# Optimization experiments

Hardware: AMD Instinct MI355X
Metric: run time of the kernel (lower is better)

The kernel has to match this reference:

```python
import jax, jax.numpy as jnp
import numpy as np

B, T, D = 64, 512, 128          # batch, time, input_dim
S = 16                           # num_sessions
P, STRIDE = 3, 1                 # patch size / stride
H = 512                          # hidden_size
HORIZONS = (1, 5, 10)
K = len(HORIZONS)
TOK = D * P                      # token_dim = 384
EPS = 1e-6


def setup_inputs() -> dict:
    key = jax.random.key(0)
    ks = jax.random.split(key, 16)
    s = 0.02
    return {
        "x": jax.random.normal(ks[0], (B, T, D), jnp.float32),
        "session_idx": jax.random.randint(ks[1], (B,), 0, S),
        # per-session affine (expert) params
        "sess_W": jax.random.normal(ks[2], (S, D, D), jnp.float32) * s,
        "sess_b": jax.random.normal(ks[3], (S, D), jnp.float32) * s,
        # projection token_dim -> hidden
        "proj_W": jax.random.normal(ks[4], (H, TOK), jnp.float32) * s,
        "proj_b": jax.random.normal(ks[5], (H,), jnp.float32) * s,
        "rms_scale": jnp.ones((H,), jnp.float32),
        # single-layer GRU params (PyTorch layout: [3H, in], gate order r,z,n)
        "gru_Wih": jax.random.normal(ks[6], (3 * H, H), jnp.float32) * s,
        "gru_Whh": jax.random.normal(ks[7], (3 * H, H), jnp.float32) * s,
        "gru_bih": jax.random.normal(ks[8], (3 * H,), jnp.float32) * s,
        "gru_bhh": jax.random.normal(ks[9], (3 * H,), jnp.float32) * s,
        # future heads (K horizons): Linear(H,H) -> GELU -> Linear(H,TOK)
        "head_W1": jax.random.normal(ks[10], (K, H, H), jnp.float32) * s,
        "head_b1": jax.random.normal(ks[11], (K, H), jnp.float32) * s,
        "head_W2": jax.random.normal(ks[12], (K, TOK, H), jnp.float32) * s,
        "head_b2": jax.random.normal(ks[13], (K, TOK), jnp.float32) * s,
    }


def _forward(x, session_idx, sess_W, sess_b, proj_W, proj_b, rms_scale,
             gru_Wih, gru_Whh, gru_bih, gru_bhh,
             head_W1, head_b1, head_W2, head_b2):
    # --- per-sample session affine (expert gather + batched GEMM) ---
    W = sess_W[session_idx]                      # [B, D, D]
    b = sess_b[session_idx]                      # [B, D]
    aligned = jnp.einsum('btd,bed->bte', x, W) + b[:, None, :]  # y = x @ W.T + b

    # --- patch unfold along time; torch unfold gives [N, D, P] -> flatten (d,p) ---
    N = (T - P) // STRIDE + 1
    idx = jnp.arange(N)[:, None] * STRIDE + jnp.arange(P)[None, :]  # [N, P]
    win = aligned[:, idx, :]                     # [B, N, P, D]
    tokens = jnp.transpose(win, (0, 1, 3, 2)).reshape(B, N, TOK)    # [B, N, D*P]

    # --- projection + RMSNorm ---
    h = tokens @ proj_W.T + proj_b               # [B, N, H]
    rms = jnp.sqrt(jnp.mean(h * h, axis=-1, keepdims=True) + EPS)
    h = h / rms * rms_scale

    # --- GRU (PyTorch gate order r, z, n) via lax.scan over time ---
    gx = h @ gru_Wih.T + gru_bih                 # [B, N, 3H], precomputed input gates
    gx_t = jnp.transpose(gx, (1, 0, 2))          # [N, B, 3H]

    def step(hprev, g):
        gh = hprev @ gru_Whh.T + gru_bhh         # [B, 3H]
        r = jax.nn.sigmoid(g[:, :H] + gh[:, :H])
        z = jax.nn.sigmoid(g[:, H:2 * H] + gh[:, H:2 * H])
        n = jnp.tanh(g[:, 2 * H:] + r * gh[:, 2 * H:])
        hn = (1.0 - z) * n + z * hprev
        return hn, hn

    h0 = jnp.zeros((B, H), h.dtype)
    _, hs = jax.lax.scan(step, h0, gx_t)         # [N, B, H]
    hidden = jnp.transpose(hs, (1, 0, 2))        # [B, N, H]

    # --- multi-head future MLPs (stacked over K horizons) ---
    a = jnp.einsum('bnh,kfh->kbnf', hidden, head_W1) + head_b1[:, None, None, :]
    a = jax.nn.gelu(a, approximate=False)        # torch nn.GELU default = exact
    preds = jnp.einsum('kbnf,ktf->kbnt', a, head_W2) + head_b2[:, None, None, :]
    return preds, tokens                          # preds: [K, B, N, TOK]


def reference(x, session_idx, sess_W, sess_b, proj_W, proj_b, rms_scale,
              gru_Wih, gru_Whh, gru_bih, gru_bhh,
              head_W1, head_b1, head_W2, head_b2):
    return _forward(x, session_idx, sess_W, sess_b, proj_W, proj_b, rms_scale,
                    gru_Wih, gru_Whh, gru_bih, gru_bhh,
                    head_W1, head_b1, head_W2, head_b2)
```

## Files before the change

kernel.cpp:

```cpp
#include <hip/hip_runtime.h>
#include <hip/hip_bf16.h>
#include <math.h>

typedef __hip_bfloat16 bf16;
typedef __attribute__((ext_vector_type(8))) short short8;
typedef __attribute__((ext_vector_type(4))) short short4v;
typedef __attribute__((ext_vector_type(4))) float f32x4;

#define B_    64
#define T_    512
#define D_    128
#define N_    510
#define H_    512
#define TOK_  384
#define PRED1_ 12533760L
#define TOKOFF_ 37601280L

#define O_XBF  0UL
#define O_SWB  8388608UL
#define O_PW   8912896UL
#define O_WIH  9306112UL
#define O_WHH  10878976UL
#define O_W1   12451840UL
#define O_W2   14024704UL
#define O_TOK  15204352UL
#define O_HBF  40271872UL
#define O_HID  73695232UL
#define O_ABF  107118592UL
#define O_GX   140541952UL

__global__ void k_f2b(const float* __restrict__ s, bf16* __restrict__ d, int n4) {
  int i = blockIdx.x * 256 + threadIdx.x;
  if (i < n4) {
    float4 v = ((const float4*)s)[i];
    union { short4v sv; bf16 h[4]; } u;
    u.h[0] = __float2bfloat16(v.x); u.h[1] = __float2bfloat16(v.y);
    u.h[2] = __float2bfloat16(v.z); u.h[3] = __float2bfloat16(v.w);
    ((short4v*)d)[i] = u.sv;
  }
}

enum { EPI_F32 = 0, EPI_BF16 = 1, EPI_GELU = 2, EPI_TOK = 3, EPI_F32R = 4 };
#define SLDA 40

template <int EPI>
__global__ __launch_bounds__(256, 2) void k_gemm(
    const bf16* __restrict__ A, const bf16* __restrict__ W,
    const float* __restrict__ bias, void* __restrict__ C,
    int K, int ldc, long zA, long zW, long zB, long zC,
    const int* __restrict__ sidx, float* __restrict__ tokf, bf16* __restrict__ tokb)
{
  const int tid = threadIdx.x;
  const int bm = blockIdx.x, bn = blockIdx.y, z = blockIdx.z;
  const int wsel = (EPI == EPI_TOK) ? sidx[z] : z;
  const int lane = tid & 63, wave = tid >> 6;
  const int wm = (wave & 1) << 6, wn = (wave >> 1) << 6;
  const int r16 = lane & 15, quad = lane >> 4;

  __shared__ bf16 sA[128 * SLDA];
  __shared__ bf16 sB[128 * SLDA];

  const bf16* Ag = A + (long)z * zA + (long)bm * 128 * K;
  const bf16* Wg = W + (long)wsel * zW + (long)bn * 128 * K;

  f32x4 zf = {0.f, 0.f, 0.f, 0.f};
  f32x4 acc[4][4];
  for (int i = 0; i < 4; ++i) for (int j = 0; j < 4; ++j) acc[i][j] = zf;

  const int sr = tid >> 1, sc = (tid & 1) << 4;
  for (int k0 = 0; k0 < K; k0 += 32) {
    *(short8*)&sA[sr*SLDA + sc]     = *(const short8*)&Ag[(long)sr*K + k0 + sc];
    *(short8*)&sA[sr*SLDA + sc + 8] = *(const short8*)&Ag[(long)sr*K + k0 + sc + 8];
    *(short8*)&sB[sr*SLDA + sc]     = *(const short8*)&Wg[(long)sr*K + k0 + sc];
    *(short8*)&sB[sr*SLDA + sc + 8] = *(const short8*)&Wg[(long)sr*K + k0 + sc + 8];
    __syncthreads();
    short8 fa[4], fb[4];
    for (int i = 0; i < 4; ++i) fa[i] = *(const short8*)&sA[(wm + i*16 + r16)*SLDA + quad*8];
    for (int j = 0; j < 4; ++j) fb[j] = *(const short8*)&sB[(wn + j*16 + r16)*SLDA + quad*8];
    for (int i = 0; i < 4; ++i)
      for (int j = 0; j < 4; ++j)
        acc[i][j] = __builtin_amdgcn_mfma_f32_16x16x32_bf16(fa[i], fb[j], acc[i][j], 0, 0, 0);
    __syncthreads();
  }

  const float* bz = bias + (long)wsel * zB + bn * 128;
  for (int i = 0; i < 4; ++i) {
    for (int j = 0; j < 4; ++j) {
      const int colL = wn + j*16 + r16;
      const float bv = bz[colL];
      for (int r = 0; r < 4; ++r) {
        float v = acc[i][j][r] + bv;
        const long grow = (long)bm*128 + wm + i*16 + quad*4 + r;
        const long gcol = (long)bn*128 + colL;
        if (EPI == EPI_F32) {
          ((float*)C)[(long)z*zC + grow*ldc + gcol] = v;
        } else if (EPI == EPI_BF16) {
          ((bf16*)C)[(long)z*zC + grow*ldc + gcol] = __float2bfloat16(v);
        } else if (EPI == EPI_GELU) {
          v = 0.5f * v * (1.0f + erff(v * 0.70710678118654752f));
          ((bf16*)C)[(long)z*zC + grow*ldc + gcol] = __float2bfloat16(v);
        } else if (EPI == EPI_F32R) {
          const long rb = grow & 63, rn = grow >> 6;
          ((float*)C)[(rb*510 + rn)*ldc + gcol] = v;
        } else {
          for (int p = 0; p < 3; ++p) {
            long n = grow - p;
            if (n >= 0 && n < N_) {
              tokf[((long)z*N_ + n)*TOK_ + gcol*3 + p] = v;
              tokb[((long)n*B_ + z)*TOK_ + gcol*3 + p] = __float2bfloat16(v);
            }
          }
        }
      }
    }
  }
}

__global__ __launch_bounds__(256) void k_rms(const float* __restrict__ hpre,
                                             const float* __restrict__ scale,
                                             bf16* __restrict__ hbf)
{
  const int wave = threadIdx.x >> 6, lane = threadIdx.x & 63;
  const long row = (long)blockIdx.x * 4 + wave;
  const float* p = hpre + row * 512 + lane * 8;
  float4 v0 = *(const float4*)p;
  float4 v1 = *(const float4*)(p + 4);
  float ss = v0.x*v0.x + v0.y*v0.y + v0.z*v0.z + v0.w*v0.w
           + v1.x*v1.x + v1.y*v1.y + v1.z*v1.z + v1.w*v1.w;
  for (int m = 32; m >= 1; m >>= 1) ss += __shfl_xor(ss, m, 64);
  const float inv = 1.0f / sqrtf(ss * (1.0f/512.0f) + 1e-6f);
  const float* sc = scale + lane * 8;
  union { short8 sv; bf16 h[8]; } u;
  u.h[0] = __float2bfloat16(v0.x*inv*sc[0]); u.h[1] = __float2bfloat16(v0.y*inv*sc[1]);
  u.h[2] = __float2bfloat16(v0.z*inv*sc[2]); u.h[3] = __float2bfloat16(v0.w*inv*sc[3]);
  u.h[4] = __float2bfloat16(v1.x*inv*sc[4]); u.h[5] = __float2bfloat16(v1.y*inv*sc[5]);
  u.h[6] = __float2bfloat16(v1.z*inv*sc[6]); u.h[7] = __float2bfloat16(v1.w*inv*sc[7]);
  *(short8*)(hbf + row * 512 + lane * 8) = u.sv;
}

#define KP 520

__global__ __launch_bounds__(64, 1) void k_gru(
    const bf16* __restrict__ gx,
    const bf16* __restrict__ Whh,
    const float* __restrict__ bhh,
    bf16* __restrict__ hidden,
    int* __restrict__ flags)
{
  const int lane = threadIdx.x & 63;
  const int c16  = lane & 15, quad = lane >> 4;
  const int pw   = blockIdx.x & 31;
  const int gb   = blockIdx.x >> 5;
  const int hwv  = pw * 16;
  const int b0   = gb * 8;

  __shared__ bf16 wlds[3 * 16 * KP];

  for (int rr = 0; rr < 48; ++rr) {
    const int g3 = rr >> 4, r = rr & 15;
    *(short8*)&wlds[(g3*16 + r)*KP + lane*8] =
        *(const short8*)&Whh[((long)(g3*512 + hwv + r))*512 + lane*8];
  }
  const float bhr = bhh[       hwv + c16];
  const float bhz = bhh[ 512 + hwv + c16];
  const float bhn = bhh[1024 + hwv + c16];
  __syncthreads();

  int* myflag = &flags[(gb*32 + pw) * 32];
  const int pidx = (gb*32 + (lane & 31)) * 32;
  const int brv = (quad & 1) * 4;

  float gr[4], gz[4], gn[4], pr[4], pz[4], pn[4];
  {
    const bf16* gxs = gx + (long)b0 * 1536 + hwv + c16;
#pragma unroll
    for (int i2 = 0; i2 < 4; ++i2) {
      const long ro = (long)(brv + i2) * 1536;
      gr[i2] = __bfloat162float(gxs[ro]);
      gz[i2] = __bfloat162float(gxs[ro + 512]);
      gn[i2] = __bfloat162float(gxs[ro + 1024]);
    }
  }

  for (int s = 0; s < 510; ++s) {
    {
      const int s1 = (s < 509) ? s + 1 : 509;
      const bf16* gxs = gx + ((long)s1*64 + b0)*1536 + hwv + c16;
#pragma unroll
      for (int i2 = 0; i2 < 4; ++i2) {
        const long ro = (long)(brv + i2) * 1536;
        pr[i2] = __bfloat162float(gxs[ro]);
        pz[i2] = __bfloat162float(gxs[ro + 512]);
        pn[i2] = __bfloat162float(gxs[ro + 1024]);
      }
    }

    f32x4 ar = {0.f,0.f,0.f,0.f}, az = {0.f,0.f,0.f,0.f}, an = {0.f,0.f,0.f,0.f};
    float hpv[4] = {0.f,0.f,0.f,0.f};

    if (s > 0) {
      while (true) {
        int fv = __hip_atomic_load(&flags[pidx], __ATOMIC_RELAXED, __HIP_MEMORY_SCOPE_AGENT);
        if (__all(fv >= s)) break;
        __builtin_amdgcn_s_sleep(1);
      }
      asm volatile("" ::: "memory");

      union { unsigned long long q[2]; short8 s8; } au[16];
      {
        const unsigned long long* hq = (const unsigned long long*)
            (hidden + ((long)(s-1)*64 + b0 + (c16 & 7)) * 512);
#pragma unroll
        for (int kt = 0; kt < 16; ++kt) {
          au[kt].q[0] = __hip_atomic_load(hq + kt*8 + quad*2,     __ATOMIC_RELAXED, __HIP_MEMORY_SCOPE_AGENT);
          au[kt].q[1] = __hip_atomic_load(hq + kt*8 + quad*2 + 1, __ATOMIC_RELAXED, __HIP_MEMORY_SCOPE_AGENT);
        }
      }
      {
        const unsigned* hpd = (const unsigned*)(hidden + ((long)(s-1)*64 + b0)*512);
#pragma unroll
        for (int i2 = 0; i2 < 4; ++i2) {
          unsigned d = __hip_atomic_load(hpd + ((long)(brv+i2)*512 + hwv + (c16 & ~1))/2,
                                         __ATOMIC_RELAXED, __HIP_MEMORY_SCOPE_AGENT);
          union { unsigned short u; bf16 h; } cb;
          cb.u = (unsigned short)((c16 & 1) ? (d >> 16) : (d & 0xffff));
          hpv[i2] = __bfloat162float(cb.h);
        }
      }
#pragma unroll
      for (int kt = 0; kt < 16; ++kt) {
        const int ko = kt*32 + quad*8;
        short8 fr = *(const short8*)&wlds[( 0 + c16)*KP + ko];
        short8 fz = *(const short8*)&wlds[(16 + c16)*KP + ko];
        short8 fn = *(const short8*)&wlds[(32 + c16)*KP + ko];
        ar = __builtin_amdgcn_mfma_f32_16x16x32_bf16(au[kt].s8, fr, ar, 0, 0, 0);
        az = __builtin_amdgcn_mfma_f32_16x16x32_bf16(au[kt].s8, fz, az, 0, 0, 0);
        an = __builtin_amdgcn_mfma_f32_16x16x32_bf16(au[kt].s8, fn, an, 0, 0, 0);
      }
    }

    if (quad < 2) {
#pragma unroll
      for (int i2 = 0; i2 < 4; ++i2) {
        const float r  = 1.0f / (1.0f + expf(-(gr[i2] + ar[i2] + bhr)));
        const float z  = 1.0f / (1.0f + expf(-(gz[i2] + az[i2] + bhz)));
        const float nn = tanhf(gn[i2] + r * (an[i2] + bhn));
        const float hn = (1.0f - z)*nn + z*hpv[i2];
        union { bf16 h; unsigned short u; } cb; cb.h = __float2bfloat16(hn);
        unsigned mine = cb.u;
        unsigned part = (unsigned)__shfl_xor((int)mine, 1, 64);
        if (!(c16 & 1)) {
          unsigned w = (part << 16) | mine;
          __hip_atomic_store((unsigned*)(hidden + ((long)s*64 + b0 + brv + i2)*512 + hwv + c16),
                             w, __ATOMIC_RELAXED, __HIP_MEMORY_SCOPE_AGENT);
        }
      }
    }
    if (s < 509) {
      asm volatile("s_waitcnt vmcnt(0)" ::: "memory");
      if (lane == 0)
        __hip_atomic_store(myflag, s + 1, __ATOMIC_RELAXED, __HIP_MEMORY_SCOPE_AGENT);
    }
#pragma unroll
    for (int i2 = 0; i2 < 4; ++i2) { gr[i2]=pr[i2]; gz[i2]=pz[i2]; gn[i2]=pn[i2]; }
  }
}

extern "C" void kernel_launch(void* const* d_in, const int* in_sizes, int n_in,
                              void* d_out, int out_size, void* d_ws, size_t ws_size,
                              hipStream_t stream)
{
  const float* x    = (const float*)d_in[0];
  const int*   sidx = (const int*)d_in[1];
  const float* sW   = (const float*)d_in[2];
  const float* sb   = (const float*)d_in[3];
  const float* pW   = (const float*)d_in[4];
  const float* pb   = (const float*)d_in[5];
  const float* rsc  = (const float*)d_in[6];
  const float* wih  = (const float*)d_in[7];
  const float* whh  = (const float*)d_in[8];
  const float* bih  = (const float*)d_in[9];
  const float* bhh  = (const float*)d_in[10];
  const float* w1   = (const float*)d_in[11];
  const float* b1   = (const float*)d_in[12];
  const float* w2   = (const float*)d_in[13];
  const float* b2   = (const float*)d_in[14];
  char* ws = (char*)d_ws;
  float* out = (float*)d_out;

  bf16* xbf   = (bf16*)(ws + O_XBF);
  bf16* swbf  = (bf16*)(ws + O_SWB);
  bf16* pwbf  = (bf16*)(ws + O_PW);
  bf16* wihbf = (bf16*)(ws + O_WIH);
  bf16* whhbf = (bf16*)(ws + O_WHH);
  bf16* w1bf  = (bf16*)(ws + O_W1);
  bf16* w2bf  = (bf16*)(ws + O_W2);
  bf16* tokbf = (bf16*)(ws + O_TOK);
  bf16* hbf   = (bf16*)(ws + O_HBF);
  bf16* hidbf = (bf16*)(ws + O_HID);
  bf16* abf   = (bf16*)(ws + O_ABF);
  int*  bar   = (int*)(ws + O_ABF);
  float* hpre = (float*)(ws + O_GX);
  bf16* gxbf  = (bf16*)(ws + O_GX);

  auto cvt = [&](const float* s, bf16* dp, long n) {
    int n4 = (int)(n >> 2);
    k_f2b<<<dim3((n4 + 255) / 256), dim3(256), 0, stream>>>(s, dp, n4);
  };
  cvt(x,   xbf,   (long)B_*T_*D_);
  cvt(sW,  swbf,  16L*128*128);
  cvt(pW,  pwbf,  512L*384);
  cvt(wih, wihbf, 1536L*512);
  cvt(whh, whhbf, 1536L*512);
  cvt(w1,  w1bf,  3L*512*512);
  cvt(w2,  w2bf,  3L*384*512);

  k_gemm<EPI_TOK><<<dim3(4, 1, 64), dim3(256), 0, stream>>>(
      xbf, swbf, sb, nullptr, 128, 0,
      (long)T_*D_, 128L*128, 128L, 0L, sidx, out + TOKOFF_, tokbf);

  k_gemm<EPI_F32><<<dim3(255, 4, 1), dim3(256), 0, stream>>>(
      tokbf, pwbf, pb, hpre, 384, 512, 0, 0, 0, 0, nullptr, nullptr, nullptr);

  k_rms<<<dim3(8160), dim3(256), 0, stream>>>(hpre, rsc, hbf);

  k_gemm<EPI_BF16><<<dim3(255, 12, 1), dim3(256), 0, stream>>>(
      hbf, wihbf, bih, gxbf, 512, 1536, 0, 0, 0, 0, nullptr, nullptr, nullptr);

  hipMemsetAsync(ws + O_ABF, 0, 32768, stream);
  k_gru<<<dim3(256), dim3(64), 0, stream>>>(gxbf, whhbf, bhh, hidbf, bar);

  for (int k = 0; k < 3; ++k) {
    k_gemm<EPI_GELU><<<dim3(255, 4, 1), dim3(256), 0, stream>>>(
        hidbf, w1bf + (long)k*512*512, b1 + (long)k*512, abf,
        512, 512, 0, 0, 0, 0, nullptr, nullptr, nullptr);
    k_gemm<EPI_F32R><<<dim3(255, 3, 1), dim3(256), 0, stream>>>(
        abf, w2bf + (long)k*384*512, b2 + (long)k*384, out + (long)k*PRED1_,
        512, 384, 0, 0, 0, 0, nullptr, nullptr, nullptr);
  }
}
```

Measured before the change: 2.617 ms.

## Pipeline GRU recurrence by waiting per producer group and keeping h in registers

The GRU step kernel now waits on producer flags in four phases of eight producer blocks each, and starts loading h chunks and issuing MFMAs as soon as each group of producers has published. Before, it waited for all 32 producers before starting. The Whh slice in LDS is laid out in fragment order, so each lane reads a contiguous short8 per k-tile and gate. The previous hidden value for each lane's own output is now carried in registers (rounded to bf16) instead of being reloaded from global memory. The aim is to overlap the cross-block wait with compute and to cut global loads on the serial critical path, at the cost of more polling branches.

```diff
diff --git a/kernel.cpp b/kernel.cpp
--- a/kernel.cpp
+++ b/kernel.cpp
@@ -138,8 +138,6 @@
   *(short8*)(hbf + row * 512 + lane * 8) = u.sv;
 }
 
-#define KP 520
-
 __global__ __launch_bounds__(64, 1) void k_gru(
     const bf16* __restrict__ gx,
     const bf16* __restrict__ Whh,
@@ -154,13 +152,12 @@
   const int hwv  = pw * 16;
   const int b0   = gb * 8;
 
-  __shared__ bf16 wlds[3 * 16 * KP];
-
-  for (int rr = 0; rr < 48; ++rr) {
-    const int g3 = rr >> 4, r = rr & 15;
-    *(short8*)&wlds[(g3*16 + r)*KP + lane*8] =
-        *(const short8*)&Whh[((long)(g3*512 + hwv + r))*512 + lane*8];
-  }
+  __shared__ bf16 wlds[16 * 3 * 64 * 8];
+
+  for (int g3 = 0; g3 < 3; ++g3)
+    for (int kt = 0; kt < 16; ++kt)
+      *(short8*)&wlds[((kt*3 + g3)*64 + lane)*8] =
+          *(const short8*)&Whh[(long)(g3*512 + hwv + c16)*512 + kt*32 + quad*8];
   const float bhr = bhh[       hwv + c16];
   const float bhz = bhh[ 512 + hwv + c16];
   const float bhn = bhh[1024 + hwv + c16];
@@ -171,6 +168,7 @@
   const int brv = (quad & 1) * 4;
 
   float gr[4], gz[4], gn[4], pr[4], pz[4], pn[4];
+  float hcur[4] = {0.f, 0.f, 0.f, 0.f};
   {
     const bf16* gxs = gx + (long)b0 * 1536 + hwv + c16;
 #pragma unroll
@@ -196,46 +194,40 @@
     }
 
     f32x4 ar = {0.f,0.f,0.f,0.f}, az = {0.f,0.f,0.f,0.f}, an = {0.f,0.f,0.f,0.f};
-    float hpv[4] = {0.f,0.f,0.f,0.f};
 
     if (s > 0) {
-      while (true) {
-        int fv = __hip_atomic_load(&flags[pidx], __ATOMIC_RELAXED, __HIP_MEMORY_SCOPE_AGENT);
-        if (__all(fv >= s)) break;
-        __builtin_amdgcn_s_sleep(1);
-      }
-      asm volatile("" ::: "memory");
-
-      union { unsigned long long q[2]; short8 s8; } au[16];
-      {
-        const unsigned long long* hq = (const unsigned long long*)
-            (hidden + ((long)(s-1)*64 + b0 + (c16 & 7)) * 512);
-#pragma unroll
-        for (int kt = 0; kt < 16; ++kt) {
-          au[kt].q[0] = __hip_atomic_load(hq + kt*8 + quad*2,     __ATOMIC_RELAXED, __HIP_MEMORY_SCOPE_AGENT);
-          au[kt].q[1] = __hip_atomic_load(hq + kt*8 + quad*2 + 1, __ATOMIC_RELAXED, __HIP_MEMORY_SCOPE_AGENT);
-        }
-      }
-      {
-        const unsigned* hpd = (const unsigned*)(hidden + ((long)(s-1)*64 + b0)*512);
-#pragma unroll
-        for (int i2 = 0; i2 < 4; ++i2) {
-          unsigned d = __hip_atomic_load(hpd + ((long)(brv+i2)*512 + hwv + (c16 & ~1))/2,
-                                         __ATOMIC_RELAXED, __HIP_MEMORY_SCOPE_AGENT);
-          union { unsigned short u; bf16 h; } cb;
-          cb.u = (unsigned short)((c16 & 1) ? (d >> 16) : (d & 0xffff));
-          hpv[i2] = __bfloat162float(cb.h);
-        }
-      }
-#pragma unroll
-      for (int kt = 0; kt < 16; ++kt) {
-        const int ko = kt*32 + quad*8;
-        short8 fr = *(const short8*)&wlds[( 0 + c16)*KP + ko];
-        short8 fz = *(const short8*)&wlds[(16 + c16)*KP + ko];
-        short8 fn = *(const short8*)&wlds[(32 + c16)*KP + ko];
-        ar = __builtin_amdgcn_mfma_f32_16x16x32_bf16(au[kt].s8, fr, ar, 0, 0, 0);
-        az = __builtin_amdgcn_mfma_f32_16x16x32_bf16(au[kt].s8, fz, az, 0, 0, 0);
-        an = __builtin_amdgcn_mfma_f32_16x16x32_bf16(au[kt].s8, fn, an, 0, 0, 0);
+      const unsigned long long* hq = (const unsigned long long*)
+          (hidden + ((long)(s-1)*64 + b0 + (c16 & 7)) * 512);
+      unsigned blv = 0;
+#pragma unroll
+      for (int ph = 0; ph < 4; ++ph) {
+        const unsigned pm = 0xFFu << (ph*8);
+        if ((blv & pm) != pm) {
+          while (true) {
+            int fv = __hip_atomic_load(&flags[pidx], __ATOMIC_RELAXED, __HIP_MEMORY_SCOPE_AGENT);
+            blv = (unsigned)__ballot(fv >= s);
+            if ((blv & pm) == pm) break;
+            __builtin_amdgcn_s_sleep(1);
+          }
+          asm volatile("" ::: "memory");
+        }
+        union { unsigned long long q[2]; short8 s8; } au4[4];
+#pragma unroll
+        for (int k4 = 0; k4 < 4; ++k4) {
+          const int kt = ph*4 + k4;
+          au4[k4].q[0] = __hip_atomic_load(hq + kt*8 + quad*2,     __ATOMIC_RELAXED, __HIP_MEMORY_SCOPE_AGENT);
+          au4[k4].q[1] = __hip_atomic_load(hq + kt*8 + quad*2 + 1, __ATOMIC_RELAXED, __HIP_MEMORY_SCOPE_AGENT);
+        }
+#pragma unroll
+        for (int k4 = 0; k4 < 4; ++k4) {
+          const int kt = ph*4 + k4;
+          short8 fr = *(const short8*)&wlds[((kt*3 + 0)*64 + lane)*8];
+          short8 fz = *(const short8*)&wlds[((kt*3 + 1)*64 + lane)*8];
+          short8 fn = *(const short8*)&wlds[((kt*3 + 2)*64 + lane)*8];
+          ar = __builtin_amdgcn_mfma_f32_16x16x32_bf16(au4[k4].s8, fr, ar, 0, 0, 0);
+          az = __builtin_amdgcn_mfma_f32_16x16x32_bf16(au4[k4].s8, fz, az, 0, 0, 0);
+          an = __builtin_amdgcn_mfma_f32_16x16x32_bf16(au4[k4].s8, fn, an, 0, 0, 0);
+        }
       }
     }
 
@@ -245,8 +237,9 @@
         const float r  = 1.0f / (1.0f + expf(-(gr[i2] + ar[i2] + bhr)));
         const float z  = 1.0f / (1.0f + expf(-(gz[i2] + az[i2] + bhz)));
         const float nn = tanhf(gn[i2] + r * (an[i2] + bhn));
-        const float hn = (1.0f - z)*nn + z*hpv[i2];
+        const float hn = (1.0f - z)*nn + z*hcur[i2];
         union { bf16 h; unsigned short u; } cb; cb.h = __float2bfloat16(hn);
+        hcur[i2] = __bfloat162float(cb.h);
         unsigned mine = cb.u;
         unsigned part = (unsigned)__shfl_xor((int)mine, 1, 64);
         if (!(c16 & 1)) {
```

Measured after the change: 2.788 ms. +6.5%, slower.
